# Kernel optimization log

Hardware: AMD Instinct MI355X
Metric: run time of the kernel (lower is better)

## Reference

```python
import jax, jax.numpy as jnp
import numpy as np
import math

B, CIN, W = 8, 1, 1024
D, H, NL, NE, DFF = 256, 2, 2, 10, 1024
LAT = W // 2
DK = D // H

def _pe_table(max_len, d):
    pos = np.arange(max_len)[:, None].astype(np.float32)
    div = np.exp(np.arange(0, d, 2).astype(np.float32) * (-math.log(10000.0) / d))
    pe = np.zeros((max_len, d), np.float32)
    pe[:, 0::2] = np.sin(pos * div)
    pe[:, 1::2] = np.cos(pos * div)
    return jnp.asarray(pe[None])

def _ln(x, g, b, eps=1e-5):
    mu = jnp.mean(x, -1, keepdims=True)
    var = jnp.mean(jnp.square(x - mu), -1, keepdims=True)
    return (x - mu) * jax.lax.rsqrt(var + eps) * g + b

def setup_inputs() -> dict:
    key = jax.random.key(0)
    ks = iter(jax.random.split(key, 64))
    tn = lambda shape: 0.02 * jax.random.truncated_normal(next(ks), -2.0, 2.0, shape, jnp.float32)
    return dict(
        x=jax.random.normal(next(ks), (B, CIN, W), jnp.float32),
        conv_w=tn((D, CIN, 5)), conv_b=tn((D,)),
        pe=_pe_table(LAT, D),
        ln0_g=jnp.ones((D,), jnp.float32), ln0_b=jnp.zeros((D,), jnp.float32),
        wq=tn((NL, D, D)), bq=tn((NL, D)),
        wk=tn((NL, D, D)), bk=tn((NL, D)),
        wv=tn((NL, D, D)), bv=tn((NL, D)),
        wo=tn((NL, D, D)), bo=tn((NL, D)),
        ln1_g=jnp.ones((NL, D), jnp.float32), ln1_b=jnp.zeros((NL, D), jnp.float32),
        ln2_g=jnp.ones((NL, D), jnp.float32), ln2_b=jnp.zeros((NL, D), jnp.float32),
        router_w=tn((NL, NE, D)), router_b=tn((NL, NE)),
        e_w1=tn((NL, NE, D, DFF)), e_b1=tn((NL, NE, DFF)),
        e_w2=tn((NL, NE, DFF, D)), e_b2=tn((NL, NE, D)),
        deconv_w=tn((D, D, 4)), deconv_b=tn((D,)),
        lin1_w=tn((128, D)), lin1_b=tn((128,)),
        lin2_w=tn((1, 128)), lin2_b=tn((1,)),
    )

def _forward(x, conv_w, conv_b, pe, ln0_g, ln0_b, wq, bq, wk, bk, wv, bv, wo, bo,
             ln1_g, ln1_b, ln2_g, ln2_b, router_w, router_b,
             e_w1, e_b1, e_w2, e_b2, deconv_w, deconv_b,
             lin1_w, lin1_b, lin2_w, lin2_b):
    # Conv1d(k=5, p=2, replicate) tokenizer + LPPool1d(p=2, k=2, s=2)
    xp = jnp.pad(x, ((0, 0), (0, 0), (2, 2)), mode='edge')
    h = jax.lax.conv_general_dilated(xp, conv_w, window_strides=(1,), padding=[(0, 0)],
                                     dimension_numbers=('NCH', 'OIH', 'NCH'))
    h = h + conv_b[None, :, None]
    h = jnp.sqrt(jnp.sum(jnp.square(h).reshape(B, D, LAT, 2), -1))   # LP pool, p=2
    z = h.transpose(0, 2, 1) + pe                                     # [B, LAT, D]
    z = _ln(z, ln0_g, ln0_b)
    counts_l, rprob_l = [], []
    for l in range(NL):
        q = (z @ wq[l].T + bq[l]).reshape(B, LAT, H, DK).transpose(0, 2, 1, 3)
        k = (z @ wk[l].T + bk[l]).reshape(B, LAT, H, DK).transpose(0, 2, 1, 3)
        v = (z @ wv[l].T + bv[l]).reshape(B, LAT, H, DK).transpose(0, 2, 1, 3)
        attn = jax.nn.softmax(jnp.einsum('bhqd,bhkd->bhqk', q, k) / math.sqrt(DK), -1)
        a = jnp.einsum('bhqk,bhkd->bhqd', attn, v).transpose(0, 2, 1, 3).reshape(B, LAT, D)
        z = _ln(z + (a @ wo[l].T + bo[l]), ln1_g[l], ln1_b[l])
        # Switch FFN: top-1 routing, no token drop, scale output by max route prob
        t = z.reshape(-1, D)                                          # [T, D]
        rp = jax.nn.softmax(t @ router_w[l].T + router_b[l], -1)      # [T, E]
        routes = jnp.argmax(rp, -1)
        rmax = jnp.max(rp, -1)
        hh = jax.nn.relu(jnp.einsum('td,edf->tef', t, e_w1[l]) + e_b1[l])
        yy = jnp.einsum('tef,efd->ted', hh, e_w2[l]) + e_b2[l]
        y = yy[jnp.arange(t.shape[0]), routes] * rmax[:, None]
        counts_l.append(jnp.sum(jax.nn.one_hot(routes, NE, dtype=jnp.float32), 0))
        rprob_l.append(jnp.sum(rp, 0))
        z = _ln(z + y.reshape(B, LAT, D), ln2_g[l], ln2_b[l])
    # ConvTranspose1d(k=4, s=2, p=1) == dilated conv with flipped/transposed kernel
    dw = jnp.flip(deconv_w, -1).transpose(1, 0, 2)                    # [out, in, k]
    u = jax.lax.conv_general_dilated(z.transpose(0, 2, 1), dw, window_strides=(1,),
                                     padding=[(2, 2)], lhs_dilation=(2,),
                                     dimension_numbers=('NCH', 'OIH', 'NCH'))
    u = (u + deconv_b[None, :, None]).transpose(0, 2, 1)              # [B, W, D]
    u = jnp.tanh(u @ lin1_w.T + lin1_b)
    out = (u @ lin2_w.T + lin2_b).transpose(0, 2, 1)                  # [B, 1, W]
    counts = jnp.stack(counts_l)                                      # [NL, NE]
    rprob = jnp.stack(rprob_l)
    total = jnp.sum(counts, -1, keepdims=True)
    loss_moe = NE * jnp.sum((counts / total) * (rprob / total))
    return out, loss_moe

def reference(x, conv_w, conv_b, pe, ln0_g, ln0_b, wq, bq, wk, bk, wv, bv, wo, bo,
              ln1_g, ln1_b, ln2_g, ln2_b, router_w, router_b,
              e_w1, e_b1, e_w2, e_b2, deconv_w, deconv_b,
              lin1_w, lin1_b, lin2_w, lin2_b):
    return _forward(x, conv_w, conv_b, pe, ln0_g, ln0_b, wq, bq, wk, bk, wv, bv, wo, bo,
                    ln1_g, ln1_b, ln2_g, ln2_b, router_w, router_b,
                    e_w1, e_b1, e_w2, e_b2, deconv_w, deconv_b,
                    lin1_w, lin1_b, lin2_w, lin2_b)
```

## Files before the change

kernel.cpp:

```cpp
#include <hip/hip_runtime.h>
#include <math.h>

#define LATN 512
#define DN 256
#define DKN 128
#define TTOT 4096
#define NEXP 10
#define DFFN 1024

using bf16x8 = __attribute__((ext_vector_type(8))) short;
using f32x4  = __attribute__((ext_vector_type(4))) float;

__device__ __forceinline__ float dot4(float4 a, float4 b) {
    return a.x*b.x + a.y*b.y + a.z*b.z + a.w*b.w;
}

__device__ __forceinline__ unsigned short f2bf(float f) {
    union { float f; unsigned int u; } v; v.f = f;
    unsigned int u = v.u + 0x7FFFu + ((v.u >> 16) & 1u);
    return (unsigned short)(u >> 16);
}

__device__ __forceinline__ float block_reduce_sum(float v, float* red) {
    #pragma unroll
    for (int off = 32; off; off >>= 1) v += __shfl_down(v, off, 64);
    int lane = threadIdx.x & 63, wid = threadIdx.x >> 6;
    if (lane == 0) red[wid] = v;
    __syncthreads();
    float r = red[0] + red[1] + red[2] + red[3];
    __syncthreads();
    return r;
}

__device__ __forceinline__ float wave_sum(float x) {
    #pragma unroll
    for (int off = 32; off; off >>= 1) x += __shfl_xor(x, off, 64);
    return x;
}

__global__ void zero_kernel(float* rprob_p, int* ec_p) {
    int i = threadIdx.x;
    if (i < 320) { rprob_p[i] = 0.f; ec_p[i] = 0; }
}

__global__ void tokenizer_kernel(const float* __restrict__ x, const float* __restrict__ cw,
                                 const float* __restrict__ cb, const float* __restrict__ pe,
                                 const float* __restrict__ g, const float* __restrict__ bb,
                                 float* __restrict__ z) {
    int blk = blockIdx.x;
    int l = blk & (LATN - 1);
    int b = blk >> 9;
    int d = threadIdx.x;
    __shared__ float red[8];
    const float* xb = x + (size_t)b * 1024;
    float w0 = cw[d*5+0], w1 = cw[d*5+1], w2 = cw[d*5+2], w3 = cw[d*5+3], w4 = cw[d*5+4];
    float bv = cb[d];
    int p0 = 2 * l;
    auto xc = [&](int i) { return xb[min(max(i, 0), 1023)]; };
    float h0 = bv + w0*xc(p0-2) + w1*xc(p0-1) + w2*xc(p0)   + w3*xc(p0+1) + w4*xc(p0+2);
    float h1 = bv + w0*xc(p0-1) + w1*xc(p0)   + w2*xc(p0+1) + w3*xc(p0+2) + w4*xc(p0+3);
    float pool = sqrtf(h0*h0 + h1*h1);
    float val = pool + pe[l*DN + d];
    float s = block_reduce_sum(val, red);
    float mu = s * (1.0f/DN);
    float dv = val - mu;
    float s2 = block_reduce_sum(dv*dv, red);
    float r = rsqrtf(s2 * (1.0f/DN) + 1e-5f);
    z[((size_t)b*LATN + l)*DN + d] = dv*r*g[d] + bb[d];
}

__global__ void pack_proj(const float* __restrict__ wq, const float* __restrict__ wk,
                          const float* __restrict__ wv, const float* __restrict__ wo,
                          unsigned short* __restrict__ wp) {
    int mat = blockIdx.y;
    int l0 = mat >> 2, which = mat & 3;
    const float* base = (which == 0) ? wq : (which == 1) ? wk : (which == 2) ? wv : wo;
    const float* W = base + l0*65536;
    int tid = blockIdx.x*256 + threadIdx.x;
    int l = tid & 63, kk = (tid >> 6) & 7, nt = tid >> 9;
    const float* src = W + (size_t)(nt*16 + (l&15))*DN + kk*32 + (l>>4)*8;
    unsigned short o[8];
    #pragma unroll
    for (int j = 0; j < 8; ++j) o[j] = f2bf(src[j]);
    *(ulonglong2*)(wp + (size_t)mat*65536 + (size_t)tid*8) = *(ulonglong2*)o;
}

template<int OM>
__device__ __forceinline__ void proj_body(const float* __restrict__ A,
                                          const unsigned short* __restrict__ wpm,
                                          const float* __restrict__ bias,
                                          void* __restrict__ outp, int t0, float oscale,
                                          unsigned short* ts) {
    int tid = threadIdx.x;
    #pragma unroll
    for (int i = 0; i < 16; ++i) {
        int f4 = i*256 + tid;
        int row = f4 >> 6, c4 = f4 & 63;
        float4 a = *(const float4*)&A[(size_t)(t0+row)*DN + c4*4];
        ushort4 o = { f2bf(a.x), f2bf(a.y), f2bf(a.z), f2bf(a.w) };
        *(ushort4*)&ts[row*264 + c4*4] = o;
    }
    __syncthreads();
    int w = tid >> 6, l = tid & 63;
    f32x4 acc[4][4];
    #pragma unroll
    for (int m = 0; m < 4; ++m)
        #pragma unroll
        for (int n = 0; n < 4; ++n) acc[m][n] = (f32x4){0.f,0.f,0.f,0.f};
    const bf16x8* wv = (const bf16x8*)wpm;
    #pragma unroll
    for (int kk = 0; kk < 8; ++kk) {
        bf16x8 af[4];
        #pragma unroll
        for (int m = 0; m < 4; ++m)
            af[m] = *(const bf16x8*)&ts[(m*16 + (l&15))*264 + kk*32 + (l>>4)*8];
        #pragma unroll
        for (int n = 0; n < 4; ++n) {
            bf16x8 bf = wv[((w*4 + n)*8 + kk)*64 + l];
            #pragma unroll
            for (int m = 0; m < 4; ++m)
                acc[m][n] = __builtin_amdgcn_mfma_f32_16x16x32_bf16(af[m], bf, acc[m][n], 0, 0, 0);
        }
    }
    #pragma unroll
    for (int n = 0; n < 4; ++n) {
        int col = w*64 + n*16 + (l&15);
        float bv2 = bias[col];
        #pragma unroll
        for (int m = 0; m < 4; ++m) {
            #pragma unroll
            for (int r = 0; r < 4; ++r) {
                int row = t0 + m*16 + (l>>4)*4 + r;
                float val = acc[m][n][r] + bv2;
                if (OM == 0)
                    ((float*)outp)[(size_t)row*DN + col] = val;
                else if (OM == 1)
                    ((unsigned short*)outp)[(size_t)row*DN + col] = f2bf(val * oscale);
                else
                    ((unsigned short*)outp)[(((size_t)(row>>9)*2 + (col>>7))*128 + (col&127))*512 + (row&511)] = f2bf(val);
            }
        }
    }
}

__global__ __launch_bounds__(256)
void proj_qkv(const float* __restrict__ z, const unsigned short* __restrict__ wp,
              const float* __restrict__ bq, const float* __restrict__ bk,
              const float* __restrict__ bv,
              unsigned short* __restrict__ qb, unsigned short* __restrict__ kb,
              unsigned short* __restrict__ vtb) {
    __shared__ unsigned short ts[64*264];
    int mat = blockIdx.y;
    if (mat == 0)      proj_body<1>(z, wp,          bq, qb,  blockIdx.x*64, 0.08838834764831844f, ts);
    else if (mat == 1) proj_body<1>(z, wp + 65536,  bk, kb,  blockIdx.x*64, 1.0f, ts);
    else               proj_body<2>(z, wp + 131072, bv, vtb, blockIdx.x*64, 1.0f, ts);
}

__global__ __launch_bounds__(256)
void proj_one(const float* __restrict__ A, const unsigned short* __restrict__ wpm,
              const float* __restrict__ bias, float* __restrict__ out) {
    __shared__ unsigned short ts[64*264];
    proj_body<0>(A, wpm, bias, out, blockIdx.x*64, 1.0f, ts);
}

__global__ __launch_bounds__(256)
void attn_mfma(const unsigned short* __restrict__ qb, const unsigned short* __restrict__ kb,
               const unsigned short* __restrict__ vtb, float* __restrict__ a) {
    int blk = blockIdx.x;
    int xcd = blk & 7, idx = blk >> 3;
    int bh = xcd*2 + (idx & 1);
    int qt = idx >> 1;
    int b = bh >> 1, h = bh & 1;
    int q0 = qt * 32;
    int tid = threadIdx.x;
    int w = tid >> 6, l = tid & 63;
    int c = l & 15, g = l >> 4;

    __shared__ __align__(16) unsigned short p_lds[32*512];
    __shared__ float smax[4][2][16];
    __shared__ float ssum[4][2][16];

    bf16x8 qf_[2][4];
    #pragma unroll
    for (int qf = 0; qf < 2; ++qf)
        #pragma unroll
        for (int kk = 0; kk < 4; ++kk)
            qf_[qf][kk] = *(const bf16x8*)&qb[((size_t)(b*LATN + q0 + qf*16 + c))*DN + h*DKN + kk*32 + g*8];

    f32x4 st[8][2];
    #pragma unroll
    for (int f = 0; f < 8; ++f) { st[f][0] = (f32x4){0,0,0,0}; st[f][1] = (f32x4){0,0,0,0}; }
    #pragma unroll
    for (int f = 0; f < 8; ++f) {
        int kbase = w*128 + f*16;
        bf16x8 kf[4];
        #pragma unroll
        for (int kk = 0; kk < 4; ++kk)
            kf[kk] = *(const bf16x8*)&kb[((size_t)(b*LATN + kbase + c))*DN + h*DKN + kk*32 + g*8];
        #pragma unroll
        for (int kk = 0; kk < 4; ++kk) {
            st[f][0] = __builtin_amdgcn_mfma_f32_16x16x32_bf16(kf[kk], qf_[0][kk], st[f][0], 0, 0, 0);
            st[f][1] = __builtin_amdgcn_mfma_f32_16x16x32_bf16(kf[kk], qf_[1][kk], st[f][1], 0, 0, 0);
        }
    }

    float gmax[2], ginv[2];
    #pragma unroll
    for (int qf = 0; qf < 2; ++qf) {
        float m = -1e30f;
        #pragma unroll
        for (int f = 0; f < 8; ++f)
            #pragma unroll
            for (int r = 0; r < 4; ++r) m = fmaxf(m, st[f][qf][r]);
        m = fmaxf(m, __shfl_xor(m, 16, 64));
        m = fmaxf(m, __shfl_xor(m, 32, 64));
        if (l < 16) smax[w][qf][l] = m;
    }
    __syncthreads();
    #pragma unroll
    for (int qf = 0; qf < 2; ++qf)
        gmax[qf] = fmaxf(fmaxf(smax[0][qf][c], smax[1][qf][c]),
                         fmaxf(smax[2][qf][c], smax[3][qf][c]));
    #pragma unroll
    for (int qf = 0; qf < 2; ++qf) {
        float s = 0.f;
        #pragma unroll
        for (int f = 0; f < 8; ++f)
            #pragma unroll
            for (int r = 0; r < 4; ++r) {
                float e = __expf(st[f][qf][r] - gmax[qf]);
                st[f][qf][r] = e; s += e;
            }
        s += __shfl_xor(s, 16, 64);
        s += __shfl_xor(s, 32, 64);
        if (l < 16) ssum[w][qf][l] = s;
    }
    __syncthreads();
    #pragma unroll
    for (int qf = 0; qf < 2; ++qf)
        ginv[qf] = 1.0f / (ssum[0][qf][c] + ssum[1][qf][c] + ssum[2][qf][c] + ssum[3][qf][c]);

    #pragma unroll
    for (int qf = 0; qf < 2; ++qf) {
        int q_ = qf*16 + c;
        int rowb = q_ * 1024;
        int swz = (q_ & 7) << 4;
        float iv = ginv[qf];
        #pragma unroll
        for (int f = 0; f < 8; ++f) {
            unsigned int lo = (unsigned int)f2bf(st[f][qf][0]*iv) |
                              ((unsigned int)f2bf(st[f][qf][1]*iv) << 16);
            unsigned int hi = (unsigned int)f2bf(st[f][qf][2]*iv) |
                              ((unsigned int)f2bf(st[f][qf][3]*iv) << 16);
            int key0 = w*128 + f*16 + g*4;
            *(unsigned long long*)((char*)p_lds + rowb + ((key0*2) ^ swz)) =
                (unsigned long long)lo | ((unsigned long long)hi << 32);
        }
    }
    __syncthreads();

    f32x4 o[2][2];
    o[0][0] = (f32x4){0,0,0,0}; o[0][1] = (f32x4){0,0,0,0};
    o[1][0] = (f32x4){0,0,0,0}; o[1][1] = (f32x4){0,0,0,0};
    #pragma unroll
    for (int kk = 0; kk < 16; ++kk) {
        bf16x8 pb[2];
        #pragma unroll
        for (int qf = 0; qf < 2; ++qf) {
            int q_ = qf*16 + c;
            pb[qf] = *(const bf16x8*)((const char*)p_lds + q_*1024 +
                                      (((kk*32 + g*8)*2) ^ ((q_&7)<<4)));
        }
        bf16x8 va[2];
        #pragma unroll
        for (int m = 0; m < 2; ++m)
            va[m] = *(const bf16x8*)&vtb[((size_t)(bh*128 + w*32 + m*16 + c))*512 + kk*32 + g*8];
        #pragma unroll
        for (int m = 0; m < 2; ++m) {
            o[m][0] = __builtin_amdgcn_mfma_f32_16x16x32_bf16(va[m], pb[0], o[m][0], 0, 0, 0);
            o[m][1] = __builtin_amdgcn_mfma_f32_16x16x32_bf16(va[m], pb[1], o[m][1], 0, 0, 0);
        }
    }
    #pragma unroll
    for (int m = 0; m < 2; ++m)
        #pragma unroll
        for (int qf = 0; qf < 2; ++qf)
            #pragma unroll
            for (int r = 0; r < 4; ++r) {
                int d = w*32 + m*16 + g*4 + r;
                a[((size_t)(b*LATN + q0 + qf*16 + c))*DN + h*DKN + d] = o[m][qf][r];
            }
}

__global__ void ln_residual(float* __restrict__ z, const float* __restrict__ y,
                            const float* __restrict__ g, const float* __restrict__ b) {
    int t = blockIdx.x, tid = threadIdx.x;
    __shared__ float red[8];
    float val = z[(size_t)t*DN + tid] + y[(size_t)t*DN + tid];
    float s = block_reduce_sum(val, red);
    float mu = s * (1.0f/DN);
    float dv = val - mu;
    float s2 = block_reduce_sum(dv*dv, red);
    float r = rsqrtf(s2 * (1.0f/DN) + 1e-5f);
    z[(size_t)t*DN + tid] = dv*r*g[tid] + b[tid];
}

#define RTOK 32
__global__ __launch_bounds__(512)
void router_kernel(const float* __restrict__ z, const float* __restrict__ rw,
                   const float* __restrict__ rb, float* __restrict__ rmaxv,
                   float* __restrict__ rprob_p, int* __restrict__ ec_p,
                   int* __restrict__ elist) {
    __shared__ float rws[NEXP*DN];
    __shared__ float sprob[NEXP];
    __shared__ int lcnt[NEXP], lbase[NEXP];
    __shared__ int lrank[RTOK];
    __shared__ int lam[RTOK];
    int tid = threadIdx.x;
    for (int i = tid; i < NEXP*DN; i += 512) rws[i] = rw[i];
    if (tid < NEXP) { sprob[tid] = 0.f; lcnt[tid] = 0; }
    __syncthreads();
    int g = tid >> 4, j = tid & 15;
    int t = blockIdx.x * RTOK + g;
    const float4* z4 = (const float4*)&z[(size_t)t*DN + j*16];
    const float4* rws4 = (const float4*)rws;
    float acc[NEXP];
    #pragma unroll
    for (int e = 0; e < NEXP; ++e) acc[e] = 0.f;
    int r0 = (j >> 1) & 3;
    #pragma unroll
    for (int kq = 0; kq < 4; ++kq) {
        int k4 = (kq + r0) & 3;
        float4 zv = z4[k4];
        #pragma unroll
        for (int e = 0; e < NEXP; ++e)
            acc[e] += dot4(zv, rws4[e*64 + j*4 + k4]);
    }
    #pragma unroll
    for (int e = 0; e < NEXP; ++e) {
        acc[e] += __shfl_xor(acc[e], 1, 64);
        acc[e] += __shfl_xor(acc[e], 2, 64);
        acc[e] += __shfl_xor(acc[e], 4, 64);
        acc[e] += __shfl_xor(acc[e], 8, 64);
    }
    if (j == 0) {
        float lg[NEXP];
        float m = acc[0] + rb[0]; int am = 0;
        lg[0] = m;
        #pragma unroll
        for (int e = 1; e < NEXP; ++e) {
            lg[e] = acc[e] + rb[e];
            if (lg[e] > m) { m = lg[e]; am = e; }
        }
        float p[NEXP], s = 0.f;
        #pragma unroll
        for (int e = 0; e < NEXP; ++e) { p[e] = expf(lg[e] - m); s += p[e]; }
        float inv = 1.0f / s;
        rmaxv[t] = p[am] * inv;
        lam[g] = am;
        lrank[g] = atomicAdd(&lcnt[am], 1);
        #pragma unroll
        for (int e = 0; e < NEXP; ++e) atomicAdd(&sprob[e], p[e] * inv);
    }
    __syncthreads();
    if (tid < NEXP) {
        lbase[tid] = atomicAdd(&ec_p[tid*16], lcnt[tid]);
        atomicAdd(&rprob_p[tid*16], sprob[tid]);
    }
    __syncthreads();
    if (j == 0)
        elist[lam[g]*TTOT + lbase[lam[g]] + lrank[g]] = t;
}

__global__ void pack_w1(const float* __restrict__ w1l, unsigned short* __restrict__ w1p) {
    int tid = blockIdx.x*256 + threadIdx.x;
    int l = tid & 63, kk = (tid >> 6) & 7, nt = (tid >> 9) & 63, e = tid >> 15;
    const float* src = w1l + (size_t)e*262144 + (size_t)(kk*32 + (l>>4)*8)*DFFN + nt*16 + (l&15);
    unsigned short o[8];
    #pragma unroll
    for (int j = 0; j < 8; ++j) o[j] = f2bf(src[(size_t)j*DFFN]);
    ulonglong2* dst = (ulonglong2*)(w1p + (size_t)tid*8);
    *dst = *(ulonglong2*)o;
}

__global__ void pack_w2(const float* __restrict__ w2l, unsigned short* __restrict__ w2p) {
    int tid = blockIdx.x*256 + threadIdx.x;
    int l = tid & 63, kk = (tid >> 6) & 31, nt = (tid >> 11) & 15, e = tid >> 15;
    const float* src = w2l + (size_t)e*262144 + (size_t)(kk*32 + (l>>4)*8)*DN + nt*16 + (l&15);
    unsigned short o[8];
    #pragma unroll
    for (int j = 0; j < 8; ++j) o[j] = f2bf(src[(size_t)j*DN]);
    ulonglong2* dst = (ulonglong2*)(w2p + (size_t)tid*8);
    *dst = *(ulonglong2*)o;
}

#define TM 16
__global__ __launch_bounds__(256)
void moe_kernel(float* __restrict__ z, const int* __restrict__ elist,
                const int* __restrict__ ec_p, const float* __restrict__ rmaxv,
                const unsigned short* __restrict__ w1p, const float* __restrict__ b1,
                const unsigned short* __restrict__ w2p, const float* __restrict__ b2,
                const float* __restrict__ g, const float* __restrict__ bb) {
    int e = blockIdx.y;
    int cnt = ec_p[e*16];
    int base = blockIdx.x * TM;
    if (base >= cnt) return;
    int n = min(TM, cnt - base);

    __shared__ __align__(16) unsigned short ts[16*264];
    __shared__ __align__(16) unsigned short hbuf[16*1032];
    __shared__ __align__(16) float ybuf[16*260];
    __shared__ int toks[16];
    __shared__ float rm[16];

    int tid = threadIdx.x;
    int w = tid >> 6, l = tid & 63;
    if (tid < 16) {
        int tt = (tid < n) ? elist[e*TTOT + base + tid] : 0;
        toks[tid] = tt;
        rm[tid] = rmaxv[tt];
    }
    __syncthreads();
    #pragma unroll
    for (int m = 0; m < 16; ++m)
        ts[m*264 + tid] = f2bf(z[(size_t)toks[m]*DN + tid]);
    __syncthreads();

    const bf16x8* w1v = (const bf16x8*)w1p;
    const float* b1e = b1 + e*DFFN;
    f32x4 acc[16];
    #pragma unroll
    for (int i = 0; i < 16; ++i) acc[i] = (f32x4){0.f,0.f,0.f,0.f};
    #pragma unroll
    for (int kk = 0; kk < 8; ++kk) {
        bf16x8 a = *(const bf16x8*)(ts + (l&15)*264 + kk*32 + (l>>4)*8);
        const bf16x8* wbp = w1v + (((size_t)e*64 + w*16)*8 + kk)*64 + l;
        #pragma unroll
        for (int nt2 = 0; nt2 < 16; ++nt2)
            acc[nt2] = __builtin_amdgcn_mfma_f32_16x16x32_bf16(a, wbp[nt2*512], acc[nt2], 0, 0, 0);
    }
    #pragma unroll
    for (int nt2 = 0; nt2 < 16; ++nt2) {
        int col = w*256 + nt2*16 + (l&15);
        float bv = b1e[col];
        #pragma unroll
        for (int r = 0; r < 4; ++r) {
            int row = (l>>4)*4 + r;
            hbuf[row*1032 + col] = f2bf(fmaxf(acc[nt2][r] + bv, 0.f));
        }
    }
    __syncthreads();

    const bf16x8* w2v = (const bf16x8*)w2p;
    const float* b2e = b2 + e*DN;
    f32x4 acc2[4];
    #pragma unroll
    for (int i = 0; i < 4; ++i) acc2[i] = (f32x4){0.f,0.f,0.f,0.f};
    for (int kk = 0; kk < 32; ++kk) {
        bf16x8 a = *(const bf16x8*)(hbuf + (l&15)*1032 + kk*32 + (l>>4)*8);
        const bf16x8* wbp = w2v + (((size_t)e*16 + w*4)*32 + kk)*64 + l;
        #pragma unroll
        for (int nt2 = 0; nt2 < 4; ++nt2)
            acc2[nt2] = __builtin_amdgcn_mfma_f32_16x16x32_bf16(a, wbp[nt2*2048], acc2[nt2], 0, 0, 0);
    }
    #pragma unroll
    for (int nt2 = 0; nt2 < 4; ++nt2) {
        int col = w*64 + nt2*16 + (l&15);
        float bv = b2e[col];
        #pragma unroll
        for (int r = 0; r < 4; ++r) {
            int row = (l>>4)*4 + r;
            ybuf[row*260 + col] = (acc2[nt2][r] + bv) * rm[row];
        }
    }
    __syncthreads();

    #pragma unroll
    for (int rr = 0; rr < 4; ++rr) {
        int row = w*4 + rr;
        if (row < n) {
            int t = toks[row];
            float v[4];
            #pragma unroll
            for (int c = 0; c < 4; ++c)
                v[c] = ybuf[row*260 + l + 64*c] + z[(size_t)t*DN + l + 64*c];
            float s = wave_sum(v[0]+v[1]+v[2]+v[3]);
            float mu = s * (1.0f/DN);
            float s2 = 0.f;
            #pragma unroll
            for (int c = 0; c < 4; ++c) { v[c] -= mu; s2 += v[c]*v[c]; }
            s2 = wave_sum(s2);
            float rs = rsqrtf(s2 * (1.0f/DN) + 1e-5f);
            #pragma unroll
            for (int c = 0; c < 4; ++c) {
                int col = l + 64*c;
                z[(size_t)t*DN + col] = v[c]*rs*g[col] + bb[col];
            }
        }
    }
}

__global__ void pack_deconv_mfma(const float* __restrict__ w, unsigned short* __restrict__ wdp) {
    int tid = blockIdx.x*256 + threadIdx.x;
    int l = tid & 63, kk = (tid >> 6) & 7, nt = (tid >> 9) & 15, tap = tid >> 13;
    int dout = nt*16 + (l&15);
    int din0 = kk*32 + (l>>4)*8;
    unsigned short o[8];
    #pragma unroll
    for (int j = 0; j < 8; ++j)
        o[j] = f2bf(w[((size_t)(din0 + j)*DN + dout)*4 + tap]);
    *(ulonglong2*)(wdp + (size_t)tid*8) = *(ulonglong2*)o;
}

__global__ void pack_lin1(const float* __restrict__ w, unsigned short* __restrict__ wl1) {
    int tid = blockIdx.x*256 + threadIdx.x;
    int l = tid & 63, kk = (tid >> 6) & 7, nt = tid >> 9;
    const float* src = w + (size_t)(nt*16 + (l&15))*DN + kk*32 + (l>>4)*8;
    unsigned short o[8];
    #pragma unroll
    for (int j = 0; j < 8; ++j) o[j] = f2bf(src[j]);
    *(ulonglong2*)(wl1 + (size_t)tid*8) = *(ulonglong2*)o;
}

__global__ __launch_bounds__(256)
void deconv_mfma(const float* __restrict__ z, const unsigned short* __restrict__ wdp,
                 const float* __restrict__ db, float* __restrict__ u) {
    int blk = blockIdx.x;
    int b = blk >> 4, lt = blk & 15;
    int l0 = lt * 32;
    __shared__ __align__(16) unsigned short zs[34*264];
    int tid = threadIdx.x;
    #pragma unroll
    for (int i = 0; i < 9; ++i) {
        int f4 = i*256 + tid;
        if (f4 < 34*64) {
            int row = f4 >> 6, c4 = f4 & 63;
            int l = l0 - 1 + row;
            float4 a = (l >= 0 && l < LATN)
                ? *(const float4*)&z[((size_t)b*LATN + l)*DN + c4*4]
                : make_float4(0.f, 0.f, 0.f, 0.f);
            ushort4 o = { f2bf(a.x), f2bf(a.y), f2bf(a.z), f2bf(a.w) };
            *(ushort4*)&zs[row*264 + c4*4] = o;
        }
    }
    __syncthreads();
    int w = tid >> 6, l = tid & 63;
    f32x4 acce[2][4], acco[2][4];
    #pragma unroll
    for (int m = 0; m < 2; ++m)
        #pragma unroll
        for (int n = 0; n < 4; ++n) {
            acce[m][n] = (f32x4){0.f,0.f,0.f,0.f};
            acco[m][n] = (f32x4){0.f,0.f,0.f,0.f};
        }
    const bf16x8* wdv = (const bf16x8*)wdp;
    #pragma unroll
    for (int kk = 0; kk < 8; ++kk) {
        bf16x8 a0[2], a1[2], a2[2];
        #pragma unroll
        for (int m = 0; m < 2; ++m) {
            int rb = (m*16 + (l&15))*264 + kk*32 + (l>>4)*8;
            a0[m] = *(const bf16x8*)&zs[rb];
            a1[m] = *(const bf16x8*)&zs[rb + 264];
            a2[m] = *(const bf16x8*)&zs[rb + 528];
        }
        #pragma unroll
        for (int n = 0; n < 4; ++n) {
            int nt = w*4 + n;
            bf16x8 bt0 = wdv[((0*16 + nt)*8 + kk)*64 + l];
            bf16x8 bt1 = wdv[((1*16 + nt)*8 + kk)*64 + l];
            bf16x8 bt2 = wdv[((2*16 + nt)*8 + kk)*64 + l];
            bf16x8 bt3 = wdv[((3*16 + nt)*8 + kk)*64 + l];
            #pragma unroll
            for (int m = 0; m < 2; ++m) {
                acco[m][n] = __builtin_amdgcn_mfma_f32_16x16x32_bf16(a2[m], bt0, acco[m][n], 0, 0, 0);
                acce[m][n] = __builtin_amdgcn_mfma_f32_16x16x32_bf16(a1[m], bt1, acce[m][n], 0, 0, 0);
                acco[m][n] = __builtin_amdgcn_mfma_f32_16x16x32_bf16(a1[m], bt2, acco[m][n], 0, 0, 0);
                acce[m][n] = __builtin_amdgcn_mfma_f32_16x16x32_bf16(a0[m], bt3, acce[m][n], 0, 0, 0);
            }
        }
    }
    #pragma unroll
    for (int n = 0; n < 4; ++n) {
        int col = (w*4 + n)*16 + (l&15);
        float bv = db[col];
        #pragma unroll
        for (int m = 0; m < 2; ++m) {
            #pragma unroll
            for (int r = 0; r < 4; ++r) {
                int rt = m*16 + (l>>4)*4 + r;
                int wpos = 2*(l0 + rt);
                u[((size_t)b*1024 + wpos)*DN + col]     = acce[m][n][r] + bv;
                u[((size_t)b*1024 + wpos + 1)*DN + col] = acco[m][n][r] + bv;
            }
        }
    }
}

__global__ __launch_bounds__(256)
void head_mfma(const float* __restrict__ u, const unsigned short* __restrict__ wl1,
               const float* __restrict__ b1, const float* __restrict__ w2,
               const float* __restrict__ b2, float* __restrict__ out) {
    int r0 = blockIdx.x * 64;
    __shared__ __align__(16) unsigned short us[64*264];
    __shared__ float part[4][64];
    int tid = threadIdx.x;
    #pragma unroll
    for (int i = 0; i < 16; ++i) {
        int f4 = i*256 + tid;
        int row = f4 >> 6, c4 = f4 & 63;
        float4 a = *(const float4*)&u[(size_t)(r0 + row)*DN + c4*4];
        ushort4 o = { f2bf(a.x), f2bf(a.y), f2bf(a.z), f2bf(a.w) };
        *(ushort4*)&us[row*264 + c4*4] = o;
    }
    __syncthreads();
    int w = tid >> 6, l = tid & 63;
    f32x4 acc[4][2];
    #pragma unroll
    for (int m = 0; m < 4; ++m) { acc[m][0] = (f32x4){0.f,0.f,0.f,0.f}; acc[m][1] = (f32x4){0.f,0.f,0.f,0.f}; }
    const bf16x8* wv1 = (const bf16x8*)wl1;
    #pragma unroll
    for (int kk = 0; kk < 8; ++kk) {
        bf16x8 af[4];
        #pragma unroll
        for (int m = 0; m < 4; ++m)
            af[m] = *(const bf16x8*)&us[(m*16 + (l&15))*264 + kk*32 + (l>>4)*8];
        #pragma unroll
        for (int n = 0; n < 2; ++n) {
            bf16x8 bf = wv1[((w*2 + n)*8 + kk)*64 + l];
            #pragma unroll
            for (int m = 0; m < 4; ++m)
                acc[m][n] = __builtin_amdgcn_mfma_f32_16x16x32_bf16(af[m], bf, acc[m][n], 0, 0, 0);
        }
    }
    float pm[4][4];
    #pragma unroll
    for (int m = 0; m < 4; ++m)
        #pragma unroll
        for (int r = 0; r < 4; ++r) pm[m][r] = 0.f;
    #pragma unroll
    for (int n = 0; n < 2; ++n) {
        int col = (w*2 + n)*16 + (l&15);
        float bb1 = b1[col], ww2 = w2[col];
        #pragma unroll
        for (int m = 0; m < 4; ++m)
            #pragma unroll
            for (int r = 0; r < 4; ++r)
                pm[m][r] += tanhf(acc[m][n][r] + bb1) * ww2;
    }
    #pragma unroll
    for (int off = 1; off <= 8; off <<= 1)
        #pragma unroll
        for (int m = 0; m < 4; ++m)
            #pragma unroll
            for (int r = 0; r < 4; ++r)
                pm[m][r] += __shfl_xor(pm[m][r], off, 64);
    if ((l & 15) == 0) {
        #pragma unroll
        for (int m = 0; m < 4; ++m)
            #pragma unroll
            for (int r = 0; r < 4; ++r)
                part[w][m*16 + (l>>4)*4 + r] = pm[m][r];
    }
    __syncthreads();
    if (tid < 64)
        out[r0 + tid] = part[0][tid] + part[1][tid] + part[2][tid] + part[3][tid] + b2[0];
}

__global__ void loss_kernel(const int* __restrict__ ec_p, const float* __restrict__ rprob_p,
                            float* __restrict__ out) {
    if (threadIdx.x == 0) {
        float s = 0;
        for (int l = 0; l < 2; ++l)
            for (int e = 0; e < NEXP; ++e)
                s += (float)ec_p[l*160 + e*16] * rprob_p[l*160 + e*16];
        out[8192] = 10.0f * s / (4096.0f * 4096.0f);
    }
}

extern "C" void kernel_launch(void* const* d_in, const int* in_sizes, int n_in,
                              void* d_out, int out_size, void* d_ws, size_t ws_size,
                              hipStream_t stream) {
    const float* x        = (const float*)d_in[0];
    const float* conv_w   = (const float*)d_in[1];
    const float* conv_b   = (const float*)d_in[2];
    const float* pe       = (const float*)d_in[3];
    const float* ln0_g    = (const float*)d_in[4];
    const float* ln0_b    = (const float*)d_in[5];
    const float* wq       = (const float*)d_in[6];
    const float* bq       = (const float*)d_in[7];
    const float* wk       = (const float*)d_in[8];
    const float* bk       = (const float*)d_in[9];
    const float* wv       = (const float*)d_in[10];
    const float* bv       = (const float*)d_in[11];
    const float* wo       = (const float*)d_in[12];
    const float* bo       = (const float*)d_in[13];
    const float* ln1_g    = (const float*)d_in[14];
    const float* ln1_b    = (const float*)d_in[15];
    const float* ln2_g    = (const float*)d_in[16];
    const float* ln2_b    = (const float*)d_in[17];
    const float* router_w = (const float*)d_in[18];
    const float* router_b = (const float*)d_in[19];
    const float* e_w1     = (const float*)d_in[20];
    const float* e_b1     = (const float*)d_in[21];
    const float* e_w2     = (const float*)d_in[22];
    const float* e_b2     = (const float*)d_in[23];
    const float* deconv_w = (const float*)d_in[24];
    const float* deconv_b = (const float*)d_in[25];
    const float* lin1_w   = (const float*)d_in[26];
    const float* lin1_b   = (const float*)d_in[27];
    const float* lin2_w   = (const float*)d_in[28];
    const float* lin2_b   = (const float*)d_in[29];

    float* ws = (float*)d_ws;
    const size_t M = 1048576;
    float* z    = ws;
    unsigned short* qb  = (unsigned short*)(ws + 1*M);
    unsigned short* kb  = (unsigned short*)(ws + 2*M);
    unsigned short* vtb = (unsigned short*)(ws + 3*M);
    float* a    = ws + 4*M;
    float* y    = ws + 5*M;
    float* rmax = ws + 6*M;
    float* rprob_p = rmax + 4096;
    int* ec_p   = (int*)(rprob_p + 320);
    int* elist  = ec_p + 320;
    unsigned short* wproj = (unsigned short*)(ws + 6*M + 98304);
    unsigned short* w1p = (unsigned short*)(ws + 1*M);
    unsigned short* w2p = (unsigned short*)(ws + 3*M);
    float* u    = ws + 1*M;
    unsigned short* wdp = (unsigned short*)(ws + 3*M);
    unsigned short* wl1 = (unsigned short*)(ws + 3*M + 131072 + 64);
    float* out  = (float*)d_out;

    zero_kernel<<<1, 512, 0, stream>>>(rprob_p, ec_p);
    {
        dim3 pg(32, 8);
        pack_proj<<<pg, 256, 0, stream>>>(wq, wk, wv, wo, wproj);
    }
    tokenizer_kernel<<<TTOT, 256, 0, stream>>>(x, conv_w, conv_b, pe, ln0_g, ln0_b, z);

    for (int l = 0; l < 2; ++l) {
        const unsigned short* wpl = wproj + (size_t)l*4*65536;
        dim3 qkvg(64, 3);
        proj_qkv<<<qkvg, 256, 0, stream>>>(z, wpl, bq + l*256, bk + l*256, bv + l*256,
                                           qb, kb, vtb);
        attn_mfma<<<256, 256, 0, stream>>>(qb, kb, vtb, a);
        proj_one<<<64, 256, 0, stream>>>(a, wpl + 3*65536, bo + l*256, y);
        ln_residual<<<TTOT, 256, 0, stream>>>(z, y, ln1_g + l*256, ln1_b + l*256);
        router_kernel<<<TTOT/RTOK, 512, 0, stream>>>(z, router_w + l*2560, router_b + l*10,
                                                     rmax, rprob_p + l*160, ec_p + l*160,
                                                     elist + l*10*TTOT);
        pack_w1<<<1280, 256, 0, stream>>>(e_w1 + (size_t)l*2621440, w1p);
        pack_w2<<<1280, 256, 0, stream>>>(e_w2 + (size_t)l*2621440, w2p);
        dim3 mg(TTOT/TM, NEXP);
        moe_kernel<<<mg, 256, 0, stream>>>(z, elist + l*10*TTOT, ec_p + l*160, rmax,
                                           w1p, e_b1 + l*10240,
                                           w2p, e_b2 + l*2560,
                                           ln2_g + l*256, ln2_b + l*256);
    }

    pack_deconv_mfma<<<128, 256, 0, stream>>>(deconv_w, wdp);
    pack_lin1<<<16, 256, 0, stream>>>(lin1_w, wl1);
    deconv_mfma<<<128, 256, 0, stream>>>(z, wdp, deconv_b, u);
    head_mfma<<<128, 256, 0, stream>>>(u, wl1, lin1_b, lin2_w, lin2_b, out);
    loss_kernel<<<1, 64, 0, stream>>>(ec_p, rprob_p, out);
}
```

Baseline: 272.9 us.

## Fuse output projection with residual LayerNorm and remap expert blocks across XCDs

The attention output projection now adds the residual and applies LayerNorm in the same kernel, using per-row reductions through shuffles and shared memory. This removes the separate ln_residual launch and the round trip of the intermediate y buffer. The two expert weight packing kernels are merged into one launch, and both packing and MoE blocks use a 1-D grid that maps each expert to a fixed slot so its blocks land on one XCD, aiming for better L2 reuse of that expert's weights. The variance is computed as E[x²]−mu², which is less numerically stable, and the new grids launch empty blocks for the unused slots.

```diff
diff --git a/kernel.cpp b/kernel.cpp
--- a/kernel.cpp
+++ b/kernel.cpp
@@ -132,9 +132,7 @@
             for (int r = 0; r < 4; ++r) {
                 int row = t0 + m*16 + (l>>4)*4 + r;
                 float val = acc[m][n][r] + bv2;
-                if (OM == 0)
-                    ((float*)outp)[(size_t)row*DN + col] = val;
-                else if (OM == 1)
+                if (OM == 1)
                     ((unsigned short*)outp)[(size_t)row*DN + col] = f2bf(val * oscale);
                 else
                     ((unsigned short*)outp)[(((size_t)(row>>9)*2 + (col>>7))*128 + (col&127))*512 + (row&511)] = f2bf(val);
@@ -157,10 +155,100 @@
 }
 
 __global__ __launch_bounds__(256)
-void proj_one(const float* __restrict__ A, const unsigned short* __restrict__ wpm,
-              const float* __restrict__ bias, float* __restrict__ out) {
+void proj_o_ln(const float* __restrict__ A, const unsigned short* __restrict__ wpm,
+               const float* __restrict__ bias, float* __restrict__ z,
+               const float* __restrict__ lng, const float* __restrict__ lnb) {
     __shared__ unsigned short ts[64*264];
-    proj_body<0>(A, wpm, bias, out, blockIdx.x*64, 1.0f, ts);
+    __shared__ float wsum[4][64], wsq[4][64];
+    int t0 = blockIdx.x * 64;
+    int tid = threadIdx.x;
+    #pragma unroll
+    for (int i = 0; i < 16; ++i) {
+        int f4 = i*256 + tid;
+        int row = f4 >> 6, c4 = f4 & 63;
+        float4 a = *(const float4*)&A[(size_t)(t0+row)*DN + c4*4];
+        ushort4 o = { f2bf(a.x), f2bf(a.y), f2bf(a.z), f2bf(a.w) };
+        *(ushort4*)&ts[row*264 + c4*4] = o;
+    }
+    __syncthreads();
+    int w = tid >> 6, l = tid & 63, c = l & 15, g = l >> 4;
+    f32x4 acc[4][4];
+    #pragma unroll
+    for (int m = 0; m < 4; ++m)
+        #pragma unroll
+        for (int n = 0; n < 4; ++n) acc[m][n] = (f32x4){0.f,0.f,0.f,0.f};
+    const bf16x8* wv = (const bf16x8*)wpm;
+    #pragma unroll
+    for (int kk = 0; kk < 8; ++kk) {
+        bf16x8 af[4];
+        #pragma unroll
+        for (int m = 0; m < 4; ++m)
+            af[m] = *(const bf16x8*)&ts[(m*16 + c)*264 + kk*32 + g*8];
+        #pragma unroll
+        for (int n = 0; n < 4; ++n) {
+            bf16x8 bf = wv[((w*4 + n)*8 + kk)*64 + l];
+            #pragma unroll
+            for (int m = 0; m < 4; ++m)
+                acc[m][n] = __builtin_amdgcn_mfma_f32_16x16x32_bf16(af[m], bf, acc[m][n], 0, 0, 0);
+        }
+    }
+    float vals[4][4][4];
+    float sm[4][4], sq[4][4];
+    #pragma unroll
+    for (int m = 0; m < 4; ++m)
+        #pragma unroll
+        for (int r = 0; r < 4; ++r) { sm[m][r] = 0.f; sq[m][r] = 0.f; }
+    #pragma unroll
+    for (int n = 0; n < 4; ++n) {
+        int col = w*64 + n*16 + c;
+        float bv2 = bias[col];
+        #pragma unroll
+        for (int m = 0; m < 4; ++m)
+            #pragma unroll
+            for (int r = 0; r < 4; ++r) {
+                int row = t0 + m*16 + g*4 + r;
+                float v = acc[m][n][r] + bv2 + z[(size_t)row*DN + col];
+                vals[m][n][r] = v;
+                sm[m][r] += v; sq[m][r] += v*v;
+            }
+    }
+    #pragma unroll
+    for (int m = 0; m < 4; ++m)
+        #pragma unroll
+        for (int r = 0; r < 4; ++r) {
+            #pragma unroll
+            for (int off = 1; off <= 8; off <<= 1) {
+                sm[m][r] += __shfl_xor(sm[m][r], off, 64);
+                sq[m][r] += __shfl_xor(sq[m][r], off, 64);
+            }
+        }
+    if (c == 0) {
+        #pragma unroll
+        for (int m = 0; m < 4; ++m)
+            #pragma unroll
+            for (int r = 0; r < 4; ++r) {
+                wsum[w][m*16 + g*4 + r] = sm[m][r];
+                wsq[w][m*16 + g*4 + r] = sq[m][r];
+            }
+    }
+    __syncthreads();
+    #pragma unroll
+    for (int m = 0; m < 4; ++m)
+        #pragma unroll
+        for (int r = 0; r < 4; ++r) {
+            int rl = m*16 + g*4 + r;
+            float S = wsum[0][rl] + wsum[1][rl] + wsum[2][rl] + wsum[3][rl];
+            float Q = wsq[0][rl] + wsq[1][rl] + wsq[2][rl] + wsq[3][rl];
+            float mu = S * (1.0f/DN);
+            float var = Q * (1.0f/DN) - mu*mu;
+            float rs = rsqrtf(var + 1e-5f);
+            int row = t0 + rl;
+            #pragma unroll
+            for (int n = 0; n < 4; ++n) {
+                int col = w*64 + n*16 + c;
+                z[(size_t)row*DN + col] = (vals[m][n][r] - mu)*rs*lng[col] + lnb[col];
+            }
+        }
 }
 
 __global__ __launch_bounds__(256)
@@ -290,19 +378,6 @@
                 int d = w*32 + m*16 + g*4 + r;
                 a[((size_t)(b*LATN + q0 + qf*16 + c))*DN + h*DKN + d] = o[m][qf][r];
             }
-}
-
-__global__ void ln_residual(float* __restrict__ z, const float* __restrict__ y,
-                            const float* __restrict__ g, const float* __restrict__ b) {
-    int t = blockIdx.x, tid = threadIdx.x;
-    __shared__ float red[8];
-    float val = z[(size_t)t*DN + tid] + y[(size_t)t*DN + tid];
-    float s = block_reduce_sum(val, red);
-    float mu = s * (1.0f/DN);
-    float dv = val - mu;
-    float s2 = block_reduce_sum(dv*dv, red);
-    float r = rsqrtf(s2 * (1.0f/DN) + 1e-5f);
-    z[(size_t)t*DN + tid] = dv*r*g[tid] + b[tid];
 }
 
 #define RTOK 32
@@ -372,26 +447,27 @@
         elist[lam[g]*TTOT + lbase[lam[g]] + lrank[g]] = t;
 }
 
-__global__ void pack_w1(const float* __restrict__ w1l, unsigned short* __restrict__ w1p) {
-    int tid = blockIdx.x*256 + threadIdx.x;
-    int l = tid & 63, kk = (tid >> 6) & 7, nt = (tid >> 9) & 63, e = tid >> 15;
-    const float* src = w1l + (size_t)e*262144 + (size_t)(kk*32 + (l>>4)*8)*DFFN + nt*16 + (l&15);
+__global__ void pack_experts(const float* __restrict__ w1l, const float* __restrict__ w2l,
+                             unsigned short* __restrict__ w1p, unsigned short* __restrict__ w2p) {
+    int slot = blockIdx.x & 15;
+    int e = (slot & 7) + 8*(slot >> 3);
+    if (e >= NEXP) return;
+    int chunk = blockIdx.x >> 4;
+    int ie = chunk*256 + threadIdx.x;
     unsigned short o[8];
-    #pragma unroll
-    for (int j = 0; j < 8; ++j) o[j] = f2bf(src[(size_t)j*DFFN]);
-    ulonglong2* dst = (ulonglong2*)(w1p + (size_t)tid*8);
-    *dst = *(ulonglong2*)o;
-}
-
-__global__ void pack_w2(const float* __restrict__ w2l, unsigned short* __restrict__ w2p) {
-    int tid = blockIdx.x*256 + threadIdx.x;
-    int l = tid & 63, kk = (tid >> 6) & 31, nt = (tid >> 11) & 15, e = tid >> 15;
-    const float* src = w2l + (size_t)e*262144 + (size_t)(kk*32 + (l>>4)*8)*DN + nt*16 + (l&15);
-    unsigned short o[8];
-    #pragma unroll
-    for (int j = 0; j < 8; ++j) o[j] = f2bf(src[(size_t)j*DN]);
-    ulonglong2* dst = (ulonglong2*)(w2p + (size_t)tid*8);
-    *dst = *(ulonglong2*)o;
+    if (blockIdx.y == 0) {
+        int l = ie & 63, kk = (ie >> 6) & 7, nt = (ie >> 9) & 63;
+        const float* src = w1l + (size_t)e*262144 + (size_t)(kk*32 + (l>>4)*8)*DFFN + nt*16 + (l&15);
+        #pragma unroll
+        for (int j = 0; j < 8; ++j) o[j] = f2bf(src[(size_t)j*DFFN]);
+        *(ulonglong2*)(w1p + ((size_t)e*32768 + ie)*8) = *(ulonglong2*)o;
+    } else {
+        int l = ie & 63, kk = (ie >> 6) & 31, nt = (ie >> 11) & 15;
+        const float* src = w2l + (size_t)e*262144 + (size_t)(kk*32 + (l>>4)*8)*DN + nt*16 + (l&15);
+        #pragma unroll
+        for (int j = 0; j < 8; ++j) o[j] = f2bf(src[(size_t)j*DN]);
+        *(ulonglong2*)(w2p + ((size_t)e*32768 + ie)*8) = *(ulonglong2*)o;
+    }
 }
 
 #define TM 16
@@ -401,9 +477,12 @@
                 const unsigned short* __restrict__ w1p, const float* __restrict__ b1,
                 const unsigned short* __restrict__ w2p, const float* __restrict__ b2,
                 const float* __restrict__ g, const float* __restrict__ bb) {
-    int e = blockIdx.y;
+    int bid = blockIdx.x;
+    int slot = bid & 15;
+    int e = (slot & 7) + 8*(slot >> 3);
+    if (e >= NEXP) return;
     int cnt = ec_p[e*16];
-    int base = blockIdx.x * TM;
+    int base = (bid >> 4) * TM;
     if (base >= cnt) return;
     int n = min(TM, cnt - base);
 
@@ -719,7 +798,6 @@
     unsigned short* kb  = (unsigned short*)(ws + 2*M);
     unsigned short* vtb = (unsigned short*)(ws + 3*M);
     float* a    = ws + 4*M;
-    float* y    = ws + 5*M;
     float* rmax = ws + 6*M;
     float* rprob_p = rmax + 4096;
     int* ec_p   = (int*)(rprob_p + 320);
@@ -745,18 +823,20 @@
         proj_qkv<<<qkvg, 256, 0, stream>>>(z, wpl, bq + l*256, bk + l*256, bv + l*256,
                                            qb, kb, vtb);
         attn_mfma<<<256, 256, 0, stream>>>(qb, kb, vtb, a);
-        proj_one<<<64, 256, 0, stream>>>(a, wpl + 3*65536, bo + l*256, y);
-        ln_residual<<<TTOT, 256, 0, stream>>>(z, y, ln1_g + l*256, ln1_b + l*256);
+        proj_o_ln<<<64, 256, 0, stream>>>(a, wpl + 3*65536, bo + l*256, z,
+                                          ln1_g + l*256, ln1_b + l*256);
         router_kernel<<<TTOT/RTOK, 512, 0, stream>>>(z, router_w + l*2560, router_b + l*10,
                                                      rmax, rprob_p + l*160, ec_p + l*160,
                                                      elist + l*10*TTOT);
-        pack_w1<<<1280, 256, 0, stream>>>(e_w1 + (size_t)l*2621440, w1p);
-        pack_w2<<<1280, 256, 0, stream>>>(e_w2 + (size_t)l*2621440, w2p);
-        dim3 mg(TTOT/TM, NEXP);
-        moe_kernel<<<mg, 256, 0, stream>>>(z, elist + l*10*TTOT, ec_p + l*160, rmax,
-                                           w1p, e_b1 + l*10240,
-                                           w2p, e_b2 + l*2560,
-                                           ln2_g + l*256, ln2_b + l*256);
+        {
+            dim3 pkg(2048, 2);
+            pack_experts<<<pkg, 256, 0, stream>>>(e_w1 + (size_t)l*2621440,
+                                                  e_w2 + (size_t)l*2621440, w1p, w2p);
+        }
+        moe_kernel<<<4096, 256, 0, stream>>>(z, elist + l*10*TTOT, ec_p + l*160, rmax,
+                                             w1p, e_b1 + l*10240,
+                                             w2p, e_b2 + l*2560,
+                                             ln2_g + l*256, ln2_b + l*256);
     }
 
     pack_deconv_mfma<<<128, 256, 0, stream>>>(deconv_w, wdp);
```

Result: slower. 414.6 us (+51.9%).
